# Performance work log

Measured on AMD Instinct MI355X. Metric: run time of the kernel, lower is better.

The kernel has to match this reference:

```python
import jax, jax.numpy as jnp
import numpy as np

N_NODES = 100000
N_EDGES = 1600000
IN_CH = 512
HID_CH = 256
OUT_CH = 32
K = 10


def setup_inputs() -> dict:
    key = jax.random.key(0)
    k_x, k_e, k_w1, k_b1, k_w2, k_b2 = jax.random.split(key, 6)
    x = jax.random.normal(k_x, (N_NODES, IN_CH), dtype=jnp.float32)
    edge_index = jax.random.randint(k_e, (2, N_EDGES), 0, N_NODES, dtype=jnp.int64)
    s1 = 1.0 / np.sqrt(IN_CH)
    s2 = 1.0 / np.sqrt(HID_CH)
    W1 = jax.random.uniform(k_w1, (IN_CH, HID_CH), jnp.float32, -s1, s1)
    b1 = jax.random.uniform(k_b1, (HID_CH,), jnp.float32, -s1, s1)
    W2 = jax.random.uniform(k_w2, (HID_CH, OUT_CH), jnp.float32, -s2, s2)
    b2 = jax.random.uniform(k_b2, (OUT_CH,), jnp.float32, -s2, s2)
    gamma = jnp.ones((K + 1,), jnp.float32) / (K + 1)
    return {"x": x, "edge_index": edge_index, "W1": W1, "b1": b1,
            "W2": W2, "b2": b2, "gamma": gamma}


def reference(x, edge_index, W1, b1, W2, b2, gamma):
    # MLP (dropout is identity in eval mode)
    h = jax.nn.relu(x @ W1 + b1) @ W2 + b2  # [N, out]
    row, col = edge_index[0], edge_index[1]
    # symmetric normalization: deg over destination nodes (col)
    deg = jax.ops.segment_sum(jnp.ones((N_EDGES,), h.dtype), col,
                              num_segments=N_NODES)
    deg_inv_sqrt = jnp.where(deg > 0, jax.lax.rsqrt(jnp.maximum(deg, 1.0)), 0.0)
    norm = (deg_inv_sqrt[row] * deg_inv_sqrt[col])[:, None]  # [E, 1]
    out = gamma[0] * h
    h_k = h
    for k in range(1, K + 1):
        # one hop: gather source feats, scale, scatter-add to destinations
        h_k = jax.ops.segment_sum(norm * h_k[row], col, num_segments=N_NODES)
        out = out + gamma[k] * h_k
    return out
```

## Files before the change

### kernel.cpp

```cpp
#include <hip/hip_runtime.h>
#include <hip/hip_bf16.h>

#define NN    100000
#define NE    1600000
#define INCH  512
#define HIDCH 256
#define OUTCH 32
#define KHOPS 10
#define NEPAD (NE + 3 * NN)
#define NBKT  8
#define BDIV  12500
#define BCAP  204800
#define EPB_A 8192
#define EPB_B 2048

typedef __attribute__((ext_vector_type(8))) short short8;
typedef __attribute__((ext_vector_type(4))) float f32x4;

#define GLOAD_LDS16(gsrc, ldst) \
  __builtin_amdgcn_global_load_lds((const __attribute__((address_space(1))) void*)(gsrc), \
                                   (__attribute__((address_space(3))) void*)(ldst), 16, 0, 0)

constexpr size_t ws_align(size_t x) { return (x + 255) & ~(size_t)255; }
constexpr size_t USZ = ws_align((size_t)(NN + 1) * 32 * 2);
constexpr size_t OFF_H1   = 0;
constexpr size_t OFF_U0   = OFF_H1   + ws_align((size_t)NN*HIDCH*2);
constexpr size_t OFF_U1   = OFF_U0   + USZ;
constexpr size_t OFF_W1TH = OFF_U1   + USZ;
constexpr size_t OFF_W1TL = OFF_W1TH + ws_align((size_t)HIDCH*INCH*2);
constexpr size_t OFF_W2TH = OFF_W1TL + ws_align((size_t)HIDCH*INCH*2);
constexpr size_t OFF_W2TL = OFF_W2TH + ws_align((size_t)OUTCH*HIDCH*2);
constexpr size_t OFF_DEG  = OFF_W2TL + ws_align((size_t)OUTCH*HIDCH*2);
constexpr size_t OFF_DIS  = OFF_DEG  + ws_align((size_t)NN*4);
constexpr size_t OFF_RP   = OFF_DIS  + ws_align((size_t)NN*4);
constexpr size_t OFF_CUR  = OFF_RP   + ws_align((size_t)(NN+1)*4);
constexpr size_t OFF_CSR  = OFF_CUR  + ws_align((size_t)NN*4);
constexpr size_t OFF_PART = OFF_CSR  + ws_align((size_t)NEPAD*4);
constexpr size_t OFF_OFFS = OFF_PART + ws_align(512);
constexpr size_t OFF_BCNT = OFF_OFFS + ws_align(512);
constexpr size_t OFF_EPK8 = OFF_BCNT + ws_align(32);

__device__ __forceinline__ unsigned short bf16_rne(float f) {
  unsigned int u = __float_as_uint(f);
  u += 0x7fffu + ((u >> 16) & 1u);
  return (unsigned short)(u >> 16);
}
__device__ __forceinline__ float bf16_to_f32(unsigned short h) {
  return __uint_as_float(((unsigned int)h) << 16);
}
__device__ __forceinline__ float bflo(unsigned int w) {
  return __uint_as_float(w << 16);
}
__device__ __forceinline__ float bfhi(unsigned int w) {
  return __uint_as_float(w & 0xffff0000u);
}

__global__ __launch_bounds__(256) void k_bucket(const int* __restrict__ ei,
                                                int* __restrict__ deg,
                                                int* __restrict__ bcnt,
                                                int2* __restrict__ epk8) {
  __shared__ int hist[NBKT], rbase[NBKT], lcur[NBKT];
  const int t = threadIdx.x;
  const int e0 = blockIdx.x * EPB_A;
  if (t < NBKT) hist[t] = 0;
  __syncthreads();
  for (int i = t; i < EPB_A; i += 256) {
    int e = e0 + i;
    if (e < NE) {
      int c = ei[NE + e];
      atomicAdd(&deg[c], 1);
      atomicAdd(&hist[c / BDIV], 1);
    }
  }
  __syncthreads();
  if (t < NBKT) {
    rbase[t] = atomicAdd(&bcnt[t], hist[t]);
    lcur[t] = 0;
  }
  __syncthreads();
  for (int i = t; i < EPB_A; i += 256) {
    int e = e0 + i;
    if (e < NE) {
      int r = ei[e], c = ei[NE + e];
      int b = c / BDIV;
      int slot = atomicAdd(&lcur[b], 1);
      epk8[(size_t)b * BCAP + rbase[b] + slot] = make_int2(r, c);
    }
  }
}

__global__ __launch_bounds__(256) void k_fill2(const int2* __restrict__ epk8,
                                               const int* __restrict__ bcnt,
                                               int* __restrict__ cur,
                                               int* __restrict__ csrc) {
  const int bucket = blockIdx.x & 7;
  const int chunk = blockIdx.x >> 3;
  const int cnt = bcnt[bucket];
  const int lo = chunk * EPB_B;
  int n = cnt - lo;
  if (n > EPB_B) n = EPB_B;
  const int2* src = epk8 + (size_t)bucket * BCAP + lo;
  for (int i = threadIdx.x; i < n; i += 256) {
    int2 rc = src[i];
    int p = atomicAdd(&cur[rc.y], 1);
    csrc[p] = rc.x;
  }
}

__global__ __launch_bounds__(256) void k_dis(const int* __restrict__ deg,
                                             float* __restrict__ dis,
                                             unsigned short* u0, unsigned short* u1) {
  int v = blockIdx.x * 256 + threadIdx.x;
  if (v < NN) {
    int d = deg[v];
    dis[v] = d > 0 ? rsqrtf((float)d) : 0.0f;
  }
  if (blockIdx.x == 0) {
    int t = threadIdx.x;
    if (t < 16)      ((unsigned int*)u0)[(size_t)NN * 16 + t] = 0;
    else if (t < 32) ((unsigned int*)u1)[(size_t)NN * 16 + (t - 16)] = 0;
  }
}

__global__ __launch_bounds__(256) void k_scan1(const int* __restrict__ deg,
                                               int* __restrict__ rp,
                                               int* __restrict__ part) {
  __shared__ int s[256];
  int b = blockIdx.x, t = threadIdx.x;
  int base = b * 1024 + t * 4;
  int v0 = (base + 0 < NN) ? ((deg[base + 0] + 3) & ~3) : 0;
  int v1 = (base + 1 < NN) ? ((deg[base + 1] + 3) & ~3) : 0;
  int v2 = (base + 2 < NN) ? ((deg[base + 2] + 3) & ~3) : 0;
  int v3 = (base + 3 < NN) ? ((deg[base + 3] + 3) & ~3) : 0;
  int tot = v0 + v1 + v2 + v3;
  s[t] = tot;
  __syncthreads();
  for (int d = 1; d < 256; d <<= 1) {
    int x = (t >= d) ? s[t - d] : 0;
    __syncthreads();
    s[t] += x;
    __syncthreads();
  }
  int excl = s[t] - tot;
  if (t == 255) part[b] = s[255];
  if (base + 0 < NN) rp[base + 0] = excl;
  if (base + 1 < NN) rp[base + 1] = excl + v0;
  if (base + 2 < NN) rp[base + 2] = excl + v0 + v1;
  if (base + 3 < NN) rp[base + 3] = excl + v0 + v1 + v2;
}

__global__ __launch_bounds__(128) void k_scan2(const int* __restrict__ part,
                                               int* __restrict__ offs) {
  __shared__ int s[128];
  int t = threadIdx.x;
  int v = (t < 98) ? part[t] : 0;
  s[t] = v;
  __syncthreads();
  for (int d = 1; d < 128; d <<= 1) {
    int x = (t >= d) ? s[t - d] : 0;
    __syncthreads();
    s[t] += x;
    __syncthreads();
  }
  if (t < 98) offs[t] = s[t] - v;
}

__global__ __launch_bounds__(256) void k_scan3(int* __restrict__ rp,
                                               const int* __restrict__ offs,
                                               const int* __restrict__ part,
                                               int* __restrict__ cur) {
  int b = blockIdx.x, t = threadIdx.x;
  int o = offs[b];
  int base = b * 1024 + t * 4;
#pragma unroll
  for (int j = 0; j < 4; ++j) {
    int i = base + j;
    if (i < NN) {
      int r = rp[i] + o;
      rp[i] = r;
      cur[i] = r;
    }
  }
  if (b == 0 && t == 0) rp[NN] = offs[97] + part[97];
}

__global__ __launch_bounds__(256) void k_pad(const int* __restrict__ cur,
                                             const int* __restrict__ rp,
                                             int* __restrict__ csrc) {
  int v = blockIdx.x * 256 + threadIdx.x;
  if (v < NN) {
    int p = cur[v], e = rp[v + 1];
    for (; p < e; ++p) csrc[p] = NN;
  }
}

__global__ __launch_bounds__(256) void k_splitT(const float* __restrict__ src,
                                                unsigned short* __restrict__ dh,
                                                unsigned short* __restrict__ dl,
                                                int K, int N) {
  int idx = blockIdx.x * 256 + threadIdx.x;
  if (idx >= K * N) return;
  int n = idx / K, k = idx - n * K;
  float v = src[(size_t)k * N + n];
  unsigned short h = bf16_rne(v);
  dh[idx] = h;
  dl[idx] = bf16_rne(v - bf16_to_f32(h));
}

__global__ __launch_bounds__(512, 2) void k_gemm1(const float* __restrict__ X,
                                                  const unsigned short* __restrict__ W1Th,
                                                  const float* __restrict__ bias1,
                                                  unsigned short* __restrict__ H1bf) {
  __shared__ __align__(16) unsigned short Ah[2][4096];
  __shared__ __align__(16) unsigned short Bh[2][8192];
  const int t = threadIdx.x;
  const int m0 = blockIdx.x * 128;
  const int w = t >> 6, lane = t & 63;
  const int wm = w >> 2, wn = w & 3;

  const int arow = t >> 2;
  const int achk = t & 3;
  int axrow = m0 + arow; if (axrow >= NN) axrow = NN - 1;
  const float* aptr = X + (size_t)axrow * INCH + achk * 8;
  int aidx = (arow >> 4) * 512 + ((arow & 15) + achk * 16) * 8;
  aidx ^= ((aidx >> 7) & 3) << 4;
  const int aroff = (lane * 8) ^ (((lane >> 4) & 3) << 4);

  const int bn0 = (w * 16) + (lane & 15);
  const int bko = (lane >> 4) * 8;
  const unsigned short* bs0 = W1Th + (size_t)bn0 * INCH + bko;
  const unsigned short* bs1 = W1Th + (size_t)(bn0 + 128) * INCH + bko;

  f32x4 acc[4][4] = {};
  float4 av0, av1;

  av0 = *(const float4*)(aptr);
  av1 = *(const float4*)(aptr + 4);
  GLOAD_LDS16(bs0, &Bh[0][w * 512]);
  GLOAD_LDS16(bs1, &Bh[0][(w + 8) * 512]);
  {
    float af[8] = {av0.x, av0.y, av0.z, av0.w, av1.x, av1.y, av1.z, av1.w};
    short8 ah;
#pragma unroll
    for (int i = 0; i < 8; ++i) {
      unsigned int u = __float_as_uint(af[i]);
      ah[i] = (short)((u + 0x7fffu + ((u >> 16) & 1u)) >> 16);
    }
    *(short8*)&Ah[0][aidx] = ah;
  }
  __syncthreads();

#pragma unroll
  for (int it = 0; it < 16; ++it) {
    const int cur = it & 1, nxt = cur ^ 1;
    const int k0 = it * 32;
    if (it < 15) {
      av0 = *(const float4*)(aptr + k0 + 32);
      av1 = *(const float4*)(aptr + k0 + 36);
      GLOAD_LDS16(bs0 + k0 + 32, &Bh[nxt][w * 512]);
      GLOAD_LDS16(bs1 + k0 + 32, &Bh[nxt][(w + 8) * 512]);
    }
    short8 afrag[4];
#pragma unroll
    for (int mf = 0; mf < 4; ++mf)
      afrag[mf] = *(const short8*)&Ah[cur][(wm * 4 + mf) * 512 + aroff];
#pragma unroll
    for (int nf = 0; nf < 4; ++nf) {
      short8 bfh = *(const short8*)&Bh[cur][(wn * 4 + nf) * 512 + lane * 8];
#pragma unroll
      for (int mf = 0; mf < 4; ++mf) {
        acc[mf][nf] = __builtin_amdgcn_mfma_f32_16x16x32_bf16(afrag[mf], bfh, acc[mf][nf], 0, 0, 0);
      }
    }
    if (it < 15) {
      float af[8] = {av0.x, av0.y, av0.z, av0.w, av1.x, av1.y, av1.z, av1.w};
      short8 ah;
#pragma unroll
      for (int i = 0; i < 8; ++i) {
        unsigned int u = __float_as_uint(af[i]);
        ah[i] = (short)((u + 0x7fffu + ((u >> 16) & 1u)) >> 16);
      }
      *(short8*)&Ah[nxt][aidx] = ah;
    }
    __syncthreads();
  }

  const int colbase = wn * 64 + (lane & 15);
  const int rowbase = m0 + wm * 64 + ((lane >> 4) << 2);
#pragma unroll
  for (int nf = 0; nf < 4; ++nf) {
    int col = colbase + nf * 16;
    float b = bias1[col];
#pragma unroll
    for (int mf = 0; mf < 4; ++mf) {
#pragma unroll
      for (int r = 0; r < 4; ++r) {
        int row = rowbase + mf * 16 + r;
        if (row < NN) {
          float h = fmaxf(acc[mf][nf][r] + b, 0.f);
          H1bf[(size_t)row * HIDCH + col] = bf16_rne(h);
        }
      }
    }
  }
}

__global__ __launch_bounds__(256) void k_gemm2(const unsigned short* __restrict__ H1bf,
                                               const unsigned short* __restrict__ W2Th,
                                               const unsigned short* __restrict__ W2Tl,
                                               const float* __restrict__ bias2,
                                               const float* __restrict__ gamma,
                                               const float* __restrict__ dis,
                                               unsigned short* __restrict__ u0,
                                               float* __restrict__ out) {
  __shared__ __align__(16) unsigned short A2[8192];
  __shared__ __align__(16) unsigned short B2h[2048], B2l[2048];
  const int t = threadIdx.x;
  const int m0 = blockIdx.x * 128;

  const int arow = t >> 1;
  int axrow = m0 + arow; if (axrow >= NN) axrow = NN - 1;
  const int akb = (t & 1) * 32;
  const unsigned short* ap = H1bf + (size_t)axrow * HIDCH + akb;
  const int abase = ((arow >> 4) * 2 + (akb >> 5)) * 512 + (arow & 15) * 8;

  const int bnr = t >> 3, bkq = (t & 7) * 8;
  const int bslot = ((bnr >> 4) * 2 + (bkq >> 5)) * 512 +
                    ((bnr & 15) + (((bkq & 31) >> 3) << 4)) * 8;
  const unsigned short* bhp = W2Th + (size_t)bnr * HIDCH + bkq;
  const unsigned short* blp = W2Tl + (size_t)bnr * HIDCH + bkq;

  const int w = t >> 6, lane = t & 63;

  f32x4 acc[2][2] = {};

  for (int k0 = 0; k0 < HIDCH; k0 += 64) {
    uint4 a0 = *(const uint4*)(ap + k0);
    uint4 a1 = *(const uint4*)(ap + k0 + 8);
    uint4 a2 = *(const uint4*)(ap + k0 + 16);
    uint4 a3 = *(const uint4*)(ap + k0 + 24);
    uint4 bh = *(const uint4*)(bhp + k0);
    uint4 bl = *(const uint4*)(blp + k0);

    __syncthreads();

    *(uint4*)&A2[abase + 0 * 128] = a0;
    *(uint4*)&A2[abase + 1 * 128] = a1;
    *(uint4*)&A2[abase + 2 * 128] = a2;
    *(uint4*)&A2[abase + 3 * 128] = a3;
    *(uint4*)&B2h[bslot] = bh;
    *(uint4*)&B2l[bslot] = bl;

    __syncthreads();

    const short8* AV  = (const short8*)A2;
    const short8* BHV = (const short8*)B2h;
    const short8* BLV = (const short8*)B2l;
#pragma unroll
    for (int k32 = 0; k32 < 2; ++k32) {
      short8 bfh[2], bfl[2];
#pragma unroll
      for (int nf = 0; nf < 2; ++nf) {
        bfh[nf] = BHV[(nf * 2 + k32) * 64 + lane];
        bfl[nf] = BLV[(nf * 2 + k32) * 64 + lane];
      }
#pragma unroll
      for (int mf = 0; mf < 2; ++mf) {
        short8 a = AV[((w * 2 + mf) * 2 + k32) * 64 + lane];
#pragma unroll
        for (int nf = 0; nf < 2; ++nf) {
          acc[mf][nf] = __builtin_amdgcn_mfma_f32_16x16x32_bf16(a, bfh[nf], acc[mf][nf], 0, 0, 0);
          acc[mf][nf] = __builtin_amdgcn_mfma_f32_16x16x32_bf16(a, bfl[nf], acc[mf][nf], 0, 0, 0);
        }
      }
    }
  }

  const float g0 = gamma[0];
  const int colb = lane & 15;
  const int rowb = m0 + w * 32 + ((lane >> 4) << 2);
  const float b2c0 = bias2[colb], b2c1 = bias2[16 + colb];
#pragma unroll
  for (int mf = 0; mf < 2; ++mf) {
#pragma unroll
    for (int r = 0; r < 4; ++r) {
      int row = rowb + mf * 16 + r;
      if (row < NN) {
        float dv = dis[row];
        float h0 = acc[mf][0][r] + b2c0;
        float h1 = acc[mf][1][r] + b2c1;
        size_t o = (size_t)row * 32 + colb;
        u0[o] = bf16_rne(dv * h0);
        u0[o + 16] = bf16_rne(dv * h1);
        out[o] = g0 * h0;
        out[o + 16] = g0 * h1;
      }
    }
  }
}

__global__ __launch_bounds__(256) void k_hop(const unsigned short* __restrict__ Uin,
                                             unsigned short* __restrict__ Uout,
                                             float* __restrict__ out,
                                             const int* __restrict__ rp,
                                             const int* __restrict__ csrc,
                                             const float* __restrict__ dis,
                                             const float* __restrict__ gamma,
                                             int k) {
  const int t = threadIdx.x;
  const int g = t >> 4;
  const int li = t & 15;
  const int v = blockIdx.x * 16 + g;
  const int s = rp[v], e = rp[v + 1];
  const unsigned int* Uin32 = (const unsigned int*)Uin;

  float ax0 = 0.f, ay0 = 0.f, ax1 = 0.f, ay1 = 0.f;
  float ax2 = 0.f, ay2 = 0.f, ax3 = 0.f, ay3 = 0.f;
  int j = s;
  for (; j + 8 <= e; j += 8) {
    int4 sa = *(const int4*)&csrc[j];
    int4 sb = *(const int4*)&csrc[j + 4];
    unsigned int w0 = Uin32[(size_t)sa.x * 16 + li];
    unsigned int w1 = Uin32[(size_t)sa.y * 16 + li];
    unsigned int w2 = Uin32[(size_t)sa.z * 16 + li];
    unsigned int w3 = Uin32[(size_t)sa.w * 16 + li];
    unsigned int w4 = Uin32[(size_t)sb.x * 16 + li];
    unsigned int w5 = Uin32[(size_t)sb.y * 16 + li];
    unsigned int w6 = Uin32[(size_t)sb.z * 16 + li];
    unsigned int w7 = Uin32[(size_t)sb.w * 16 + li];
    ax0 += bflo(w0); ay0 += bfhi(w0);
    ax1 += bflo(w1); ay1 += bfhi(w1);
    ax2 += bflo(w2); ay2 += bfhi(w2);
    ax3 += bflo(w3); ay3 += bfhi(w3);
    ax0 += bflo(w4); ay0 += bfhi(w4);
    ax1 += bflo(w5); ay1 += bfhi(w5);
    ax2 += bflo(w6); ay2 += bfhi(w6);
    ax3 += bflo(w7); ay3 += bfhi(w7);
  }
  if (j < e) {
    int4 sa = *(const int4*)&csrc[j];
    unsigned int w0 = Uin32[(size_t)sa.x * 16 + li];
    unsigned int w1 = Uin32[(size_t)sa.y * 16 + li];
    unsigned int w2 = Uin32[(size_t)sa.z * 16 + li];
    unsigned int w3 = Uin32[(size_t)sa.w * 16 + li];
    ax0 += bflo(w0); ay0 += bfhi(w0);
    ax1 += bflo(w1); ay1 += bfhi(w1);
    ax2 += bflo(w2); ay2 += bfhi(w2);
    ax3 += bflo(w3); ay3 += bfhi(w3);
  }
  const float Sx = (ax0 + ax1) + (ax2 + ax3);
  const float Sy = (ay0 + ay1) + (ay2 + ay3);
  const float dv = dis[v];
  const float gd = gamma[k] * dv;
  const float d2 = dv * dv;
  unsigned int packed = (unsigned int)bf16_rne(d2 * Sx) |
                        ((unsigned int)bf16_rne(d2 * Sy) << 16);
  ((unsigned int*)Uout)[(size_t)v * 16 + li] = packed;
  const size_t o = (size_t)v * 32 + li * 2;
  float2 po = *(const float2*)&out[o];
  po.x = fmaf(gd, Sx, po.x);
  po.y = fmaf(gd, Sy, po.y);
  *(float2*)&out[o] = po;
}

extern "C" void kernel_launch(void* const* d_in, const int* in_sizes, int n_in,
                              void* d_out, int out_size, void* d_ws, size_t ws_size,
                              hipStream_t stream) {
  const float* x     = (const float*)d_in[0];
  const int*   ei    = (const int*)d_in[1];
  const float* W1    = (const float*)d_in[2];
  const float* b1    = (const float*)d_in[3];
  const float* W2    = (const float*)d_in[4];
  const float* b2    = (const float*)d_in[5];
  const float* gamma = (const float*)d_in[6];
  float* out = (float*)d_out;

  char* ws = (char*)d_ws;
  unsigned short* h1bf = (unsigned short*)(ws + OFF_H1);
  unsigned short* U[2] = {(unsigned short*)(ws + OFF_U0),
                          (unsigned short*)(ws + OFF_U1)};
  unsigned short* w1th = (unsigned short*)(ws + OFF_W1TH);
  unsigned short* w1tl = (unsigned short*)(ws + OFF_W1TL);
  unsigned short* w2th = (unsigned short*)(ws + OFF_W2TH);
  unsigned short* w2tl = (unsigned short*)(ws + OFF_W2TL);
  int*   deg  = (int*)(ws + OFF_DEG);
  float* dis  = (float*)(ws + OFF_DIS);
  int*   rp   = (int*)(ws + OFF_RP);
  int*   cur  = (int*)(ws + OFF_CUR);
  int*   csrc = (int*)(ws + OFF_CSR);
  int*   part = (int*)(ws + OFF_PART);
  int*   offs = (int*)(ws + OFF_OFFS);
  int*   bcnt = (int*)(ws + OFF_BCNT);
  int2*  epk8 = (int2*)(ws + OFF_EPK8);

  hipMemsetAsync(deg, 0, NN * sizeof(int), stream);
  hipMemsetAsync(bcnt, 0, NBKT * sizeof(int), stream);

  k_splitT<<<(INCH * HIDCH + 255) / 256, 256, 0, stream>>>(W1, w1th, w1tl, INCH, HIDCH);
  k_splitT<<<(HIDCH * OUTCH + 255) / 256, 256, 0, stream>>>(W2, w2th, w2tl, HIDCH, OUTCH);

  k_bucket<<<(NE + EPB_A - 1) / EPB_A, 256, 0, stream>>>(ei, deg, bcnt, epk8);
  k_dis<<<(NN + 255) / 256, 256, 0, stream>>>(deg, dis, U[0], U[1]);
  k_scan1<<<98, 256, 0, stream>>>(deg, rp, part);
  k_scan2<<<1, 128, 0, stream>>>(part, offs);
  k_scan3<<<98, 256, 0, stream>>>(rp, offs, part, cur);
  k_fill2<<<(BCAP / EPB_B) * NBKT, 256, 0, stream>>>(epk8, bcnt, cur, csrc);
  k_pad<<<(NN + 255) / 256, 256, 0, stream>>>(cur, rp, csrc);

  k_gemm1<<<(NN + 127) / 128, 512, 0, stream>>>(x, w1th, b1, h1bf);
  k_gemm2<<<(NN + 127) / 128, 256, 0, stream>>>(h1bf, w2th, w2tl, b2, gamma, dis,
                                                U[0], out);

  for (int k = 1; k <= KHOPS; ++k) {
    k_hop<<<NN / 16, 256, 0, stream>>>(U[(k - 1) & 1], U[k & 1], out,
                                       rp, csrc, dis, gamma, k);
  }
}
```

Measured before the change: 527.7 us.

## Renumber nodes by degree bin and defer output accumulation to one merge pass

Nodes are sorted into bins by padded degree with a counting sort, and the CSR, the propagated features and the per-node scalars are renumbered into that order. Each wavefront in the hop kernel then handles nodes of similar degree, which is meant to cut load imbalance and divergence. The hop kernel no longer reads and writes the fp32 output; all ten hop results are kept in separate buffers and a single merge kernel adds them into the output at the end. This costs several extra setup kernels, about ten times the feature-buffer memory, and gathers over the permuted node order.

Result: no change. 523.7 us (-0.8%).

```diff
diff --git a/kernel.cpp b/kernel.cpp
--- a/kernel.cpp
+++ b/kernel.cpp
@@ -23,22 +23,30 @@
 
 constexpr size_t ws_align(size_t x) { return (x + 255) & ~(size_t)255; }
 constexpr size_t USZ = ws_align((size_t)(NN + 1) * 32 * 2);
-constexpr size_t OFF_H1   = 0;
-constexpr size_t OFF_U0   = OFF_H1   + ws_align((size_t)NN*HIDCH*2);
-constexpr size_t OFF_U1   = OFF_U0   + USZ;
-constexpr size_t OFF_W1TH = OFF_U1   + USZ;
-constexpr size_t OFF_W1TL = OFF_W1TH + ws_align((size_t)HIDCH*INCH*2);
-constexpr size_t OFF_W2TH = OFF_W1TL + ws_align((size_t)HIDCH*INCH*2);
-constexpr size_t OFF_W2TL = OFF_W2TH + ws_align((size_t)OUTCH*HIDCH*2);
-constexpr size_t OFF_DEG  = OFF_W2TL + ws_align((size_t)OUTCH*HIDCH*2);
-constexpr size_t OFF_DIS  = OFF_DEG  + ws_align((size_t)NN*4);
-constexpr size_t OFF_RP   = OFF_DIS  + ws_align((size_t)NN*4);
-constexpr size_t OFF_CUR  = OFF_RP   + ws_align((size_t)(NN+1)*4);
-constexpr size_t OFF_CSR  = OFF_CUR  + ws_align((size_t)NN*4);
-constexpr size_t OFF_PART = OFF_CSR  + ws_align((size_t)NEPAD*4);
-constexpr size_t OFF_OFFS = OFF_PART + ws_align(512);
-constexpr size_t OFF_BCNT = OFF_OFFS + ws_align(512);
-constexpr size_t OFF_EPK8 = OFF_BCNT + ws_align(32);
+constexpr size_t USH = USZ / 2;
+constexpr size_t OFF_H1    = 0;
+constexpr size_t OFF_U0    = OFF_H1    + ws_align((size_t)NN*HIDCH*2);
+constexpr size_t OFF_W1TH  = OFF_U0    + 11 * USZ;
+constexpr size_t OFF_W1TL  = OFF_W1TH  + ws_align((size_t)HIDCH*INCH*2);
+constexpr size_t OFF_W2TH  = OFF_W1TL  + ws_align((size_t)HIDCH*INCH*2);
+constexpr size_t OFF_W2TL  = OFF_W2TH  + ws_align((size_t)OUTCH*HIDCH*2);
+constexpr size_t OFF_DEG   = OFF_W2TL  + ws_align((size_t)OUTCH*HIDCH*2);
+constexpr size_t OFF_DIS   = OFF_DEG   + ws_align((size_t)NN*4);
+constexpr size_t OFF_RP    = OFF_DIS   + ws_align((size_t)NN*4);
+constexpr size_t OFF_CUR   = OFF_RP    + ws_align((size_t)(NN+1)*4);
+constexpr size_t OFF_NAP   = OFF_CUR   + ws_align((size_t)NN*4);
+constexpr size_t OFF_POSV  = OFF_NAP   + ws_align((size_t)NN*4);
+constexpr size_t OFF_PDGP  = OFF_POSV  + ws_align((size_t)NN*4);
+constexpr size_t OFF_D2P   = OFF_PDGP  + ws_align((size_t)NN*4);
+constexpr size_t OFF_DSQP  = OFF_D2P   + ws_align((size_t)NN*4);
+constexpr size_t OFF_CSR   = OFF_DSQP  + ws_align((size_t)NN*4);
+constexpr size_t OFF_PART  = OFF_CSR   + ws_align((size_t)NEPAD*4);
+constexpr size_t OFF_OFFS  = OFF_PART  + ws_align(512);
+constexpr size_t OFF_BCNT  = OFF_OFFS  + ws_align(512);
+constexpr size_t OFF_BINH  = OFF_BCNT  + ws_align(32);
+constexpr size_t OFF_BINO  = OFF_BINH  + ws_align(256);
+constexpr size_t OFF_BINC  = OFF_BINO  + ws_align(256);
+constexpr size_t OFF_EPK8  = OFF_BINC  + ws_align(256);
 
 __device__ __forceinline__ unsigned short bf16_rne(float f) {
   unsigned int u = __float_as_uint(f);
@@ -89,8 +97,165 @@
   }
 }
 
+__global__ __launch_bounds__(256) void k_dis(const int* __restrict__ deg,
+                                             float* __restrict__ dis,
+                                             unsigned short* __restrict__ u0) {
+  int v = blockIdx.x * 256 + threadIdx.x;
+  if (v < NN) {
+    int d = deg[v];
+    dis[v] = d > 0 ? rsqrtf((float)d) : 0.0f;
+  }
+  if (blockIdx.x == 0 && threadIdx.x < 160) {
+    int tab = threadIdx.x >> 4, li = threadIdx.x & 15;
+    ((unsigned int*)(u0 + (size_t)tab * USH))[(size_t)NN * 16 + li] = 0;
+  }
+}
+
+__global__ __launch_bounds__(256) void k_hist(const int* __restrict__ deg,
+                                              int* __restrict__ binh) {
+  __shared__ int h[64];
+  const int t = threadIdx.x;
+  if (t < 64) h[t] = 0;
+  __syncthreads();
+  int v = blockIdx.x * 256 + t;
+  if (v < NN) {
+    int bin = ((deg[v] + 3) & ~3) >> 2;
+    if (bin > 63) bin = 63;
+    atomicAdd(&h[bin], 1);
+  }
+  __syncthreads();
+  if (t < 64 && h[t]) atomicAdd(&binh[t], h[t]);
+}
+
+__global__ __launch_bounds__(64) void k_binscan(const int* __restrict__ binh,
+                                                int* __restrict__ bino,
+                                                int* __restrict__ binc) {
+  __shared__ int s[64];
+  int t = threadIdx.x;
+  int v = binh[t];
+  s[t] = v;
+  __syncthreads();
+  for (int d = 1; d < 64; d <<= 1) {
+    int x = (t >= d) ? s[t - d] : 0;
+    __syncthreads();
+    s[t] += x;
+    __syncthreads();
+  }
+  bino[t] = s[t] - v;
+  binc[t] = s[t] - v;
+}
+
+__global__ __launch_bounds__(256) void k_place(const int* __restrict__ deg,
+                                               int* __restrict__ binc,
+                                               int* __restrict__ nap,
+                                               int* __restrict__ posv,
+                                               int* __restrict__ pdgp) {
+  __shared__ int h[64], rb[64], lc[64];
+  const int t = threadIdx.x;
+  if (t < 64) h[t] = 0;
+  __syncthreads();
+  int v = blockIdx.x * 256 + t;
+  int pdeg = 0, bin = 0;
+  bool valid = v < NN;
+  if (valid) {
+    pdeg = (deg[v] + 3) & ~3;
+    bin = pdeg >> 2;
+    if (bin > 63) bin = 63;
+    atomicAdd(&h[bin], 1);
+  }
+  __syncthreads();
+  if (t < 64) {
+    rb[t] = h[t] ? atomicAdd(&binc[t], h[t]) : 0;
+    lc[t] = 0;
+  }
+  __syncthreads();
+  if (valid) {
+    int slot = atomicAdd(&lc[bin], 1);
+    int pos = rb[bin] + slot;
+    nap[pos] = v;
+    posv[v] = pos;
+    pdgp[pos] = pdeg;
+  }
+}
+
+__global__ __launch_bounds__(256) void k_scan1(const int* __restrict__ pdgp,
+                                               int* __restrict__ rp,
+                                               int* __restrict__ part) {
+  __shared__ int s[256];
+  int b = blockIdx.x, t = threadIdx.x;
+  int base = b * 1024 + t * 4;
+  int v0 = (base + 0 < NN) ? pdgp[base + 0] : 0;
+  int v1 = (base + 1 < NN) ? pdgp[base + 1] : 0;
+  int v2 = (base + 2 < NN) ? pdgp[base + 2] : 0;
+  int v3 = (base + 3 < NN) ? pdgp[base + 3] : 0;
+  int tot = v0 + v1 + v2 + v3;
+  s[t] = tot;
+  __syncthreads();
+  for (int d = 1; d < 256; d <<= 1) {
+    int x = (t >= d) ? s[t - d] : 0;
+    __syncthreads();
+    s[t] += x;
+    __syncthreads();
+  }
+  int excl = s[t] - tot;
+  if (t == 255) part[b] = s[255];
+  if (base + 0 < NN) rp[base + 0] = excl;
+  if (base + 1 < NN) rp[base + 1] = excl + v0;
+  if (base + 2 < NN) rp[base + 2] = excl + v0 + v1;
+  if (base + 3 < NN) rp[base + 3] = excl + v0 + v1 + v2;
+}
+
+__global__ __launch_bounds__(128) void k_scan2(const int* __restrict__ part,
+                                               int* __restrict__ offs) {
+  __shared__ int s[128];
+  int t = threadIdx.x;
+  int v = (t < 98) ? part[t] : 0;
+  s[t] = v;
+  __syncthreads();
+  for (int d = 1; d < 128; d <<= 1) {
+    int x = (t >= d) ? s[t - d] : 0;
+    __syncthreads();
+    s[t] += x;
+    __syncthreads();
+  }
+  if (t < 98) offs[t] = s[t] - v;
+}
+
+__global__ __launch_bounds__(256) void k_scan3(int* __restrict__ rp,
+                                               const int* __restrict__ offs,
+                                               const int* __restrict__ part) {
+  int b = blockIdx.x, t = threadIdx.x;
+  int o = offs[b];
+  int base = b * 1024 + t * 4;
+#pragma unroll
+  for (int j = 0; j < 4; ++j) {
+    int i = base + j;
+    if (i < NN) rp[i] += o;
+  }
+  if (b == 0 && t == 0) rp[NN] = offs[97] + part[97];
+}
+
+__global__ __launch_bounds__(256) void k_curinit(const int* __restrict__ nap,
+                                                 const int* __restrict__ rp,
+                                                 const int* __restrict__ deg,
+                                                 const float* __restrict__ dis,
+                                                 int* __restrict__ cur,
+                                                 float* __restrict__ d2p,
+                                                 float* __restrict__ dsqp) {
+  int p = blockIdx.x * 256 + threadIdx.x;
+  if (p < NN) {
+    int v = nap[p];
+    cur[v] = rp[p];
+    float dv = dis[v];
+    d2p[p] = dv * dv;
+    int d = deg[v];
+    dsqp[p] = d > 0 ? sqrtf((float)d) : 0.0f;
+  }
+}
+
 __global__ __launch_bounds__(256) void k_fill2(const int2* __restrict__ epk8,
                                                const int* __restrict__ bcnt,
+                                               const int* __restrict__ posv,
                                                int* __restrict__ cur,
                                                int* __restrict__ csrc) {
   const int bucket = blockIdx.x & 7;
@@ -103,94 +268,19 @@
   for (int i = threadIdx.x; i < n; i += 256) {
     int2 rc = src[i];
     int p = atomicAdd(&cur[rc.y], 1);
-    csrc[p] = rc.x;
-  }
-}
-
-__global__ __launch_bounds__(256) void k_dis(const int* __restrict__ deg,
-                                             float* __restrict__ dis,
-                                             unsigned short* u0, unsigned short* u1) {
-  int v = blockIdx.x * 256 + threadIdx.x;
-  if (v < NN) {
-    int d = deg[v];
-    dis[v] = d > 0 ? rsqrtf((float)d) : 0.0f;
-  }
-  if (blockIdx.x == 0) {
-    int t = threadIdx.x;
-    if (t < 16)      ((unsigned int*)u0)[(size_t)NN * 16 + t] = 0;
-    else if (t < 32) ((unsigned int*)u1)[(size_t)NN * 16 + (t - 16)] = 0;
-  }
-}
-
-__global__ __launch_bounds__(256) void k_scan1(const int* __restrict__ deg,
-                                               int* __restrict__ rp,
-                                               int* __restrict__ part) {
-  __shared__ int s[256];
-  int b = blockIdx.x, t = threadIdx.x;
-  int base = b * 1024 + t * 4;
-  int v0 = (base + 0 < NN) ? ((deg[base + 0] + 3) & ~3) : 0;
-  int v1 = (base + 1 < NN) ? ((deg[base + 1] + 3) & ~3) : 0;
-  int v2 = (base + 2 < NN) ? ((deg[base + 2] + 3) & ~3) : 0;
-  int v3 = (base + 3 < NN) ? ((deg[base + 3] + 3) & ~3) : 0;
-  int tot = v0 + v1 + v2 + v3;
-  s[t] = tot;
-  __syncthreads();
-  for (int d = 1; d < 256; d <<= 1) {
-    int x = (t >= d) ? s[t - d] : 0;
-    __syncthreads();
-    s[t] += x;
-    __syncthreads();
-  }
-  int excl = s[t] - tot;
-  if (t == 255) part[b] = s[255];
-  if (base + 0 < NN) rp[base + 0] = excl;
-  if (base + 1 < NN) rp[base + 1] = excl + v0;
-  if (base + 2 < NN) rp[base + 2] = excl + v0 + v1;
-  if (base + 3 < NN) rp[base + 3] = excl + v0 + v1 + v2;
-}
-
-__global__ __launch_bounds__(128) void k_scan2(const int* __restrict__ part,
-                                               int* __restrict__ offs) {
-  __shared__ int s[128];
-  int t = threadIdx.x;
-  int v = (t < 98) ? part[t] : 0;
-  s[t] = v;
-  __syncthreads();
-  for (int d = 1; d < 128; d <<= 1) {
-    int x = (t >= d) ? s[t - d] : 0;
-    __syncthreads();
-    s[t] += x;
-    __syncthreads();
-  }
-  if (t < 98) offs[t] = s[t] - v;
-}
-
-__global__ __launch_bounds__(256) void k_scan3(int* __restrict__ rp,
-                                               const int* __restrict__ offs,
-                                               const int* __restrict__ part,
-                                               int* __restrict__ cur) {
-  int b = blockIdx.x, t = threadIdx.x;
-  int o = offs[b];
-  int base = b * 1024 + t * 4;
-#pragma unroll
-  for (int j = 0; j < 4; ++j) {
-    int i = base + j;
-    if (i < NN) {
-      int r = rp[i] + o;
-      rp[i] = r;
-      cur[i] = r;
-    }
-  }
-  if (b == 0 && t == 0) rp[NN] = offs[97] + part[97];
-}
-
-__global__ __launch_bounds__(256) void k_pad(const int* __restrict__ cur,
+    csrc[p] = posv[rc.x];
+  }
+}
+
+__global__ __launch_bounds__(256) void k_pad(const int* __restrict__ nap,
+                                             const int* __restrict__ cur,
                                              const int* __restrict__ rp,
                                              int* __restrict__ csrc) {
-  int v = blockIdx.x * 256 + threadIdx.x;
-  if (v < NN) {
-    int p = cur[v], e = rp[v + 1];
-    for (; p < e; ++p) csrc[p] = NN;
+  int p = blockIdx.x * 256 + threadIdx.x;
+  if (p < NN) {
+    int v = nap[p];
+    int q = cur[v], e = rp[p + 1];
+    for (; q < e; ++q) csrc[q] = NN;
   }
 }
 
@@ -311,6 +401,7 @@
                                                const float* __restrict__ bias2,
                                                const float* __restrict__ gamma,
                                                const float* __restrict__ dis,
+                                               const int* __restrict__ posv,
                                                unsigned short* __restrict__ u0,
                                                float* __restrict__ out) {
   __shared__ __align__(16) unsigned short A2[8192];
@@ -389,9 +480,10 @@
         float dv = dis[row];
         float h0 = acc[mf][0][r] + b2c0;
         float h1 = acc[mf][1][r] + b2c1;
+        size_t op = (size_t)posv[row] * 32 + colb;
+        u0[op] = bf16_rne(dv * h0);
+        u0[op + 16] = bf16_rne(dv * h1);
         size_t o = (size_t)row * 32 + colb;
-        u0[o] = bf16_rne(dv * h0);
-        u0[o + 16] = bf16_rne(dv * h1);
         out[o] = g0 * h0;
         out[o + 16] = g0 * h1;
       }
@@ -401,17 +493,14 @@
 
 __global__ __launch_bounds__(256) void k_hop(const unsigned short* __restrict__ Uin,
                                              unsigned short* __restrict__ Uout,
-                                             float* __restrict__ out,
                                              const int* __restrict__ rp,
                                              const int* __restrict__ csrc,
-                                             const float* __restrict__ dis,
-                                             const float* __restrict__ gamma,
-                                             int k) {
+                                             const float* __restrict__ d2p) {
   const int t = threadIdx.x;
   const int g = t >> 4;
   const int li = t & 15;
-  const int v = blockIdx.x * 16 + g;
-  const int s = rp[v], e = rp[v + 1];
+  const int p = blockIdx.x * 16 + g;
+  const int s = rp[p], e = rp[p + 1];
   const unsigned int* Uin32 = (const unsigned int*)Uin;
 
   float ax0 = 0.f, ay0 = 0.f, ax1 = 0.f, ay1 = 0.f;
@@ -450,17 +539,32 @@
   }
   const float Sx = (ax0 + ax1) + (ax2 + ax3);
   const float Sy = (ay0 + ay1) + (ay2 + ay3);
-  const float dv = dis[v];
-  const float gd = gamma[k] * dv;
-  const float d2 = dv * dv;
+  const float d2 = d2p[p];
   unsigned int packed = (unsigned int)bf16_rne(d2 * Sx) |
                         ((unsigned int)bf16_rne(d2 * Sy) << 16);
-  ((unsigned int*)Uout)[(size_t)v * 16 + li] = packed;
+  ((unsigned int*)Uout)[(size_t)p * 16 + li] = packed;
+}
+
+__global__ __launch_bounds__(256) void k_merge(const unsigned short* __restrict__ u1,
+                                               const int* __restrict__ nap,
+                                               const float* __restrict__ dsqp,
+                                               const float* __restrict__ gamma,
+                                               float* __restrict__ out) {
+  const int idx = blockIdx.x * 256 + threadIdx.x;
+  const int p = idx >> 4;
+  const int li = idx & 15;
+  const int v = nap[p];
+  const float f = dsqp[p];
   const size_t o = (size_t)v * 32 + li * 2;
-  float2 po = *(const float2*)&out[o];
-  po.x = fmaf(gd, Sx, po.x);
-  po.y = fmaf(gd, Sy, po.y);
-  *(float2*)&out[o] = po;
+  float2 acc = *(const float2*)&out[o];
+#pragma unroll
+  for (int k = 0; k < KHOPS; ++k) {
+    unsigned int w = ((const unsigned int*)(u1 + (size_t)k * USH))[(size_t)p * 16 + li];
+    float gk = gamma[k + 1] * f;
+    acc.x = fmaf(gk, bflo(w), acc.x);
+    acc.y = fmaf(gk, bfhi(w), acc.y);
+  }
+  *(float2*)&out[o] = acc;
 }
 
 extern "C" void kernel_launch(void* const* d_in, const int* in_sizes, int n_in,
@@ -477,8 +581,7 @@
 
   char* ws = (char*)d_ws;
   unsigned short* h1bf = (unsigned short*)(ws + OFF_H1);
-  unsigned short* U[2] = {(unsigned short*)(ws + OFF_U0),
-                          (unsigned short*)(ws + OFF_U1)};
+  unsigned short* u0   = (unsigned short*)(ws + OFF_U0);
   unsigned short* w1th = (unsigned short*)(ws + OFF_W1TH);
   unsigned short* w1tl = (unsigned short*)(ws + OFF_W1TL);
   unsigned short* w2th = (unsigned short*)(ws + OFF_W2TH);
@@ -487,32 +590,48 @@
   float* dis  = (float*)(ws + OFF_DIS);
   int*   rp   = (int*)(ws + OFF_RP);
   int*   cur  = (int*)(ws + OFF_CUR);
+  int*   nap  = (int*)(ws + OFF_NAP);
+  int*   posv = (int*)(ws + OFF_POSV);
+  int*   pdgp = (int*)(ws + OFF_PDGP);
+  float* d2p  = (float*)(ws + OFF_D2P);
+  float* dsqp = (float*)(ws + OFF_DSQP);
   int*   csrc = (int*)(ws + OFF_CSR);
   int*   part = (int*)(ws + OFF_PART);
   int*   offs = (int*)(ws + OFF_OFFS);
   int*   bcnt = (int*)(ws + OFF_BCNT);
+  int*   binh = (int*)(ws + OFF_BINH);
+  int*   bino = (int*)(ws + OFF_BINO);
+  int*   binc = (int*)(ws + OFF_BINC);
   int2*  epk8 = (int2*)(ws + OFF_EPK8);
 
   hipMemsetAsync(deg, 0, NN * sizeof(int), stream);
   hipMemsetAsync(bcnt, 0, NBKT * sizeof(int), stream);
+  hipMemsetAsync(binh, 0, 64 * sizeof(int), stream);
 
   k_splitT<<<(INCH * HIDCH + 255) / 256, 256, 0, stream>>>(W1, w1th, w1tl, INCH, HIDCH);
   k_splitT<<<(HIDCH * OUTCH + 255) / 256, 256, 0, stream>>>(W2, w2th, w2tl, HIDCH, OUTCH);
 
   k_bucket<<<(NE + EPB_A - 1) / EPB_A, 256, 0, stream>>>(ei, deg, bcnt, epk8);
-  k_dis<<<(NN + 255) / 256, 256, 0, stream>>>(deg, dis, U[0], U[1]);
-  k_scan1<<<98, 256, 0, stream>>>(deg, rp, part);
+  k_dis<<<(NN + 255) / 256, 256, 0, stream>>>(deg, dis, u0);
+  k_hist<<<(NN + 255) / 256, 256, 0, stream>>>(deg, binh);
+  k_binscan<<<1, 64, 0, stream>>>(binh, bino, binc);
+  k_place<<<(NN + 255) / 256, 256, 0, stream>>>(deg, binc, nap, posv, pdgp);
+  k_scan1<<<98, 256, 0, stream>>>(pdgp, rp, part);
   k_scan2<<<1, 128, 0, stream>>>(part, offs);
-  k_scan3<<<98, 256, 0, stream>>>(rp, offs, part, cur);
-  k_fill2<<<(BCAP / EPB_B) * NBKT, 256, 0, stream>>>(epk8, bcnt, cur, csrc);
-  k_pad<<<(NN + 255) / 256, 256, 0, stream>>>(cur, rp, csrc);
+  k_scan3<<<98, 256, 0, stream>>>(rp, offs, part);
+  k_curinit<<<(NN + 255) / 256, 256, 0, stream>>>(nap, rp, deg, dis, cur, d2p, dsqp);
+  k_fill2<<<(BCAP / EPB_B) * NBKT, 256, 0, stream>>>(epk8, bcnt, posv, cur, csrc);
+  k_pad<<<(NN + 255) / 256, 256, 0, stream>>>(nap, cur, rp, csrc);
 
   k_gemm1<<<(NN + 127) / 128, 512, 0, stream>>>(x, w1th, b1, h1bf);
   k_gemm2<<<(NN + 127) / 128, 256, 0, stream>>>(h1bf, w2th, w2tl, b2, gamma, dis,
-                                                U[0], out);
+                                                posv, u0, out);
 
   for (int k = 1; k <= KHOPS; ++k) {
-    k_hop<<<NN / 16, 256, 0, stream>>>(U[(k - 1) & 1], U[k & 1], out,
-                                       rp, csrc, dis, gamma, k);
-  }
-}
+    unsigned short* uin  = u0 + (size_t)(k - 1) * USH;
+    unsigned short* uout = u0 + (size_t)k * USH;
+    k_hop<<<NN / 16, 256, 0, stream>>>(uin, uout, rp, csrc, d2p);
+  }
+
+  k_merge<<<NN * 16 / 256, 256, 0, stream>>>(u0 + USH, nap, dsqp, gamma, out);
+}
```
